# Performance work log

Hardware: AMD Instinct MI355X
Metric: run time of the kernel (lower is better)

Reference implementation:

```python
import jax, jax.numpy as jnp
import numpy as np

N = 4096   # number of observations
Q = 1024   # number of spatial locations (dist_matrix side)


def setup_inputs() -> dict:
    key = jax.random.key(0)
    k1, k2, k3, k4 = jax.random.split(key, 4)
    y_true = jax.random.normal(k1, (N, 1), dtype=jnp.float32)
    y_pred = jax.random.normal(k2, (N, 1), dtype=jnp.float32)
    Z_idx = jax.random.randint(k3, (N, 1), 0, Q).astype(jnp.int64)
    # symmetric distance matrix from random 2D coordinates
    coords = jax.random.uniform(k4, (Q, 2), dtype=jnp.float32) * 10.0
    diff = coords[:, None, :] - coords[None, :, :]
    dist_matrix = jnp.sqrt(jnp.sum(diff * diff, axis=-1) + 1e-12)
    sig2e = jnp.asarray(1.0, dtype=jnp.float32)
    sig2bs = jnp.ones((2,), dtype=jnp.float32)
    return {"y_true": y_true, "y_pred": y_pred, "Z_idx": Z_idx,
            "dist_matrix": dist_matrix, "sig2e": sig2e, "sig2bs": sig2bs}


def reference(y_true, y_pred, Z_idx, dist_matrix, sig2e, sig2bs):
    # NLL for the 'spatial' mixed-effects mode (custom_loss_lm).
    # V = sig2e*I + Z D Z^T with Z the one-hot indicator of Z_idx and
    # D[a,b] = sig2bs[0]*exp(-dist[a,b]/(2*sig2bs[1])).
    # Z D Z^T for one-hot Z is simply the row/col gather D[idx][:, idx],
    # which avoids materializing the dense N x Q indicator matrix.
    n = y_true.shape[0]
    idx = Z_idx[:, 0]
    D = sig2bs[0] * jnp.exp(-dist_matrix / (2.0 * sig2bs[1]))   # (Q, Q)
    V = sig2e * jnp.eye(n, dtype=jnp.float32) + D[idx][:, idx]  # (N, N)
    r = y_true - y_pred                                          # (N, 1)
    V_inv_r = jnp.linalg.solve(V, r)                             # (N, 1)
    quad = jnp.sum(r * V_inv_r)
    _, logdet = jnp.linalg.slogdet(V)
    log2pi = jnp.asarray(np.log(2.0 * np.pi), dtype=jnp.float32)
    total_loss = 0.5 * n * log2pi + 0.5 * logdet + 0.5 * quad
    return total_loss
```

## Files before the change

### kernel.cpp

```cpp
#include <hip/hip_runtime.h>
#include <math.h>

#define NN 4096
#define QQ 1024
#define LDA 1032
#define AF (1025 * 1032)

__global__ void k_stats(const float* __restrict__ yt, const float* __restrict__ yp,
                        const int* __restrict__ idx, float* __restrict__ s,
                        int* __restrict__ c, float* __restrict__ scal) {
    int i = blockIdx.x * 256 + threadIdx.x;
    float r = yt[i] - yp[i];
    int q = idx[i];
    atomicAdd(&s[q], r);
    atomicAdd(&c[q], 1);
    float v = r * r;
    for (int o = 32; o > 0; o >>= 1) v += __shfl_down(v, o, 64);
    __shared__ float red[4];
    int lane = threadIdx.x & 63, wid = threadIdx.x >> 6;
    if (lane == 0) red[wid] = v;
    __syncthreads();
    if (threadIdx.x == 0) atomicAdd(&scal[0], red[0] + red[1] + red[2] + red[3]);
}

__global__ void k_matvec(const float* __restrict__ dist, const float* __restrict__ s,
                         const int* __restrict__ c, float* __restrict__ t,
                         float* __restrict__ w, float* __restrict__ sqc,
                         float* __restrict__ scal, const float* __restrict__ sbs) {
    int i = blockIdx.x;
    float sb0 = sbs[0];
    float inv2 = 1.0f / (2.0f * sbs[1]);
    const float* dr = dist + (size_t)i * QQ;
    float acc = 0.f;
    for (int j = threadIdx.x; j < QQ; j += 256)
        acc += __expf(-dr[j] * inv2) * s[j];
    for (int o = 32; o > 0; o >>= 1) acc += __shfl_down(acc, o, 64);
    __shared__ float red[4];
    int lane = threadIdx.x & 63, wid = threadIdx.x >> 6;
    if (lane == 0) red[wid] = acc;
    __syncthreads();
    if (threadIdx.x == 0) {
        float tot = (red[0] + red[1] + red[2] + red[3]) * sb0;
        t[i] = tot;
        float sq = sqrtf((float)c[i]);
        sqc[i] = sq;
        w[i] = sq * tot;
        atomicAdd(&scal[1], s[i] * tot);
    }
}

__global__ void k_build(const float* __restrict__ dist, const float* __restrict__ sqc,
                        const float* __restrict__ w, float* __restrict__ A,
                        const float* __restrict__ se_p, const float* __restrict__ sbs) {
    int i = blockIdx.x;
    if (i == QQ) {
        for (int j = threadIdx.x; j < QQ; j += 256) A[(size_t)QQ * LDA + j] = w[j];
        return;
    }
    float sb0 = sbs[0];
    float inv2 = 1.0f / (2.0f * sbs[1]);
    float inv_se = 1.0f / se_p[0];
    float qi = sqc[i] * inv_se * sb0;
    const float* dr = dist + (size_t)i * QQ;
    float* ar = A + (size_t)i * LDA;
    for (int j = threadIdx.x; j < QQ; j += 256)
        ar[j] = ((i == j) ? 1.0f : 0.0f) + qi * sqc[j] * __expf(-dr[j] * inv2);
}

__global__ __launch_bounds__(256) void k_potrf(float* __restrict__ A, int p) {
    __shared__ float col[2][64];
    int tid = threadIdx.x;
    int i = tid & 63;
    int q = tid >> 6;
    float* base = A + (size_t)(p * 64 + i) * LDA + p * 64 + 16 * q;
    float x[16];
#pragma unroll
    for (int m4 = 0; m4 < 4; ++m4) {
        float4 v = ((const float4*)base)[m4];
        x[4 * m4 + 0] = v.x; x[4 * m4 + 1] = v.y;
        x[4 * m4 + 2] = v.z; x[4 * m4 + 3] = v.w;
    }
#pragma unroll
    for (int qk = 0; qk < 4; ++qk) {
#pragma unroll
        for (int ck = 0; ck < 16; ++ck) {
            const int k = qk * 16 + ck;
            const int b = k & 1;
            if (q == qk) {
                float xk = x[ck];
                float diag = __shfl(xk, k, 64);
                float rs = rsqrtf(diag);
                float l = (i == k) ? diag * rs : xk * rs;
                if (i >= k) x[ck] = l;
                col[b][i] = l;
            }
            __syncthreads();
            if (16 * q + 15 > k) {
                if (i > k) {
                    float li = col[b][i];
                    float cl[16];
#pragma unroll
                    for (int m4 = 0; m4 < 4; ++m4) {
                        float4 v = ((const float4*)(&col[b][16 * q]))[m4];
                        cl[4 * m4 + 0] = v.x; cl[4 * m4 + 1] = v.y;
                        cl[4 * m4 + 2] = v.z; cl[4 * m4 + 3] = v.w;
                    }
#pragma unroll
                    for (int m = 0; m < 16; ++m)
                        if (16 * q + m > k) x[m] = fmaf(-li, cl[m], x[m]);
                }
            }
        }
    }
#pragma unroll
    for (int m4 = 0; m4 < 4; ++m4)
        ((float4*)base)[m4] = make_float4(x[4 * m4 + 0], x[4 * m4 + 1],
                                          x[4 * m4 + 2], x[4 * m4 + 3]);
}

template<int K, int M>
struct TAcc {
    static __device__ __forceinline__ void run(const float (&Lb)[64][65], const float (&x)[64],
                                               float& a0, float& a1) {
        if constexpr (M < K)     a0 = fmaf(-Lb[K][M], x[M], a0);
        if constexpr (M + 1 < K) a1 = fmaf(-Lb[K][M + 1], x[M + 1], a1);
        if constexpr (M + 2 < K) TAcc<K, M + 2>::run(Lb, x, a0, a1);
    }
};
template<int K>
struct TStep {
    static __device__ __forceinline__ void run(const float (&Lb)[64][65], const float (&dinv)[64],
                                               float (&x)[64]) {
        if constexpr (K < 64) {
            float a0 = x[K], a1 = 0.f;
            TAcc<K, 0>::run(Lb, x, a0, a1);
            x[K] = (a0 + a1) * dinv[K];
            TStep<K + 1>::run(Lb, dinv, x);
        }
    }
};

__global__ __launch_bounds__(64, 2) void k_trsm(float* __restrict__ A, int p) {
    __shared__ float Lb[64][65];
    __shared__ float dinv[64];
    int t = threadIdx.x;
    const float* db = A + (size_t)(p * 64) * (LDA + 1);
    for (int i = 0; i < 64; ++i) Lb[i][t] = db[(size_t)i * LDA + t];
    dinv[t] = 1.0f / Lb[t][t];
    __syncthreads();
    int r = (p + 1) * 64 + blockIdx.x * 64 + t;
    if (r <= QQ) {
        float* ar = A + (size_t)r * LDA + p * 64;
        float x[64];
#pragma unroll
        for (int jj = 0; jj < 16; ++jj) {
            float4 v = ((const float4*)ar)[jj];
            x[4 * jj] = v.x; x[4 * jj + 1] = v.y; x[4 * jj + 2] = v.z; x[4 * jj + 3] = v.w;
        }
        TStep<0>::run(Lb, dinv, x);
#pragma unroll
        for (int jj = 0; jj < 16; ++jj)
            ((float4*)ar)[jj] = make_float4(x[4 * jj], x[4 * jj + 1], x[4 * jj + 2], x[4 * jj + 3]);
    }
}

__global__ void k_syrk(float* __restrict__ A, int p) {
    int t0 = (p + 1) * 64;
    int r0 = t0 + blockIdx.y * 32;
    int c0 = t0 + blockIdx.x * 32;
    if (c0 > r0 + 31) return;
    __shared__ float Pr[32][65];
    __shared__ float Pc[32][65];
    int t = threadIdx.x;
    int pc0 = p * 64;
    for (int idx2 = t; idx2 < 2048; idx2 += 256) {
        int i = idx2 >> 6, k = idx2 & 63;
        int rr = r0 + i;
        Pr[i][k] = (rr <= QQ) ? A[(size_t)rr * LDA + pc0 + k] : 0.f;
        int cc = c0 + i;
        Pc[i][k] = (cc < QQ) ? A[(size_t)cc * LDA + pc0 + k] : 0.f;
    }
    __syncthreads();
    int tx = t & 31, ty = t >> 5;
    float acc[4] = {0.f, 0.f, 0.f, 0.f};
#pragma unroll 4
    for (int k = 0; k < 64; ++k) {
        float b = Pc[tx][k];
#pragma unroll
        for (int ii = 0; ii < 4; ++ii)
            acc[ii] = fmaf(Pr[ty + 8 * ii][k], b, acc[ii]);
    }
#pragma unroll
    for (int ii = 0; ii < 4; ++ii) {
        int rr = r0 + ty + 8 * ii, cc = c0 + tx;
        if (rr <= QQ && cc < QQ)
            A[(size_t)rr * LDA + cc] -= acc[ii];
    }
}

__global__ void k_final(const float* __restrict__ A, const float* __restrict__ scal,
                        const float* __restrict__ se_p, float* __restrict__ out) {
    int i = threadIdx.x;
    float v1 = 2.0f * __logf(A[(size_t)i * LDA + i]);
    float yv = A[(size_t)QQ * LDA + i];
    float v2 = yv * yv;
    for (int o = 32; o > 0; o >>= 1) {
        v1 += __shfl_down(v1, o, 64);
        v2 += __shfl_down(v2, o, 64);
    }
    __shared__ float r1[16], r2[16];
    int lane = i & 63, wid = i >> 6;
    if (lane == 0) { r1[wid] = v1; r2[wid] = v2; }
    __syncthreads();
    if (i == 0) {
        float ld = 0.f, yy = 0.f;
        for (int k = 0; k < 16; ++k) { ld += r1[k]; yy += r2[k]; }
        float se = se_p[0], inv = 1.0f / se;
        float rr = scal[0], st = scal[1];
        float quad = rr * inv - inv * inv * (st - inv * yy);
        float logdetV = (float)NN * __logf(se) + ld;
        out[0] = 0.5f * (float)NN * 1.8378770664093453f + 0.5f * logdetV + 0.5f * quad;
    }
}

extern "C" void kernel_launch(void* const* d_in, const int* in_sizes, int n_in,
                              void* d_out, int out_size, void* d_ws, size_t ws_size,
                              hipStream_t stream) {
    const float* yt   = (const float*)d_in[0];
    const float* yp   = (const float*)d_in[1];
    const int*   idx  = (const int*)d_in[2];
    const float* dist = (const float*)d_in[3];
    const float* se   = (const float*)d_in[4];
    const float* sbs  = (const float*)d_in[5];
    float* out = (float*)d_out;

    float* W    = (float*)d_ws;
    float* A    = W;
    int*   c    = (int*)(W + AF);
    float* s    = W + AF + 1024;
    float* scal = W + AF + 2048;
    float* t    = scal + 2;
    float* w    = t + 1024;
    float* sqc  = w + 1024;

    hipMemsetAsync(c, 0, (1024 + 1024 + 2) * sizeof(float), stream);

    k_stats<<<dim3(NN / 256), dim3(256), 0, stream>>>(yt, yp, idx, s, c, scal);
    k_matvec<<<dim3(QQ), dim3(256), 0, stream>>>(dist, s, c, t, w, sqc, scal, sbs);
    k_build<<<dim3(QQ + 1), dim3(256), 0, stream>>>(dist, sqc, w, A, se, sbs);

    for (int p = 0; p < 16; ++p) {
        k_potrf<<<dim3(1), dim3(256), 0, stream>>>(A, p);
        int rows = (QQ + 1) - (p + 1) * 64;
        k_trsm<<<dim3((rows + 63) / 64), dim3(64), 0, stream>>>(A, p);
        int cols = QQ - (p + 1) * 64;
        if (cols > 0) {
            dim3 g((cols + 31) / 32, (rows + 31) / 32);
            k_syrk<<<g, dim3(256), 0, stream>>>(A, p);
        }
    }
    k_final<<<dim3(1), dim3(1024), 0, stream>>>(A, scal, se, out);
}
```

Before: 796.9 us.

## Fuse next diagonal Cholesky factorization into SYRK update and enlarge SYRK tiles

```diff
diff --git a/kernel.cpp b/kernel.cpp
--- a/kernel.cpp
+++ b/kernel.cpp
@@ -67,55 +67,60 @@
         ar[j] = ((i == j) ? 1.0f : 0.0f) + qi * sqc[j] * __expf(-dr[j] * inv2);
 }
 
-__global__ __launch_bounds__(256) void k_potrf(float* __restrict__ A, int p) {
-    __shared__ float col[2][64];
-    int tid = threadIdx.x;
-    int i = tid & 63;
-    int q = tid >> 6;
-    float* base = A + (size_t)(p * 64 + i) * LDA + p * 64 + 16 * q;
-    float x[16];
-#pragma unroll
-    for (int m4 = 0; m4 < 4; ++m4) {
-        float4 v = ((const float4*)base)[m4];
-        x[4 * m4 + 0] = v.x; x[4 * m4 + 1] = v.y;
-        x[4 * m4 + 2] = v.z; x[4 * m4 + 3] = v.w;
-    }
+__device__ __forceinline__ void potrf64_run(float (&x)[16], int i, int q,
+                                            float2 (&col2)[2][64]) {
 #pragma unroll
     for (int qk = 0; qk < 4; ++qk) {
 #pragma unroll
-        for (int ck = 0; ck < 16; ++ck) {
-            const int k = qk * 16 + ck;
-            const int b = k & 1;
+        for (int c2 = 0; c2 < 8; ++c2) {
+            const int k = qk * 16 + 2 * c2;
+            const int ck = 2 * c2;
+            const int b = c2 & 1;
             if (q == qk) {
                 float xk = x[ck];
-                float diag = __shfl(xk, k, 64);
-                float rs = rsqrtf(diag);
-                float l = (i == k) ? diag * rs : xk * rs;
-                if (i >= k) x[ck] = l;
-                col[b][i] = l;
+                float d0 = __shfl(xk, k, 64);
+                float rs0 = rsqrtf(d0);
+                float l0 = (i == k) ? d0 * rs0 : xk * rs0;
+                if (i >= k) x[ck] = l0;
+                float lk1 = __shfl(l0, k + 1, 64);
+                float x1v = fmaf(-l0, lk1, x[ck + 1]);
+                float d1 = __shfl(x1v, k + 1, 64);
+                float rs1 = rsqrtf(d1);
+                float l1 = (i == k + 1) ? d1 * rs1 : x1v * rs1;
+                if (i >= k + 1) x[ck + 1] = l1;
+                col2[b][i] = make_float2(l0, l1);
             }
             __syncthreads();
-            if (16 * q + 15 > k) {
-                if (i > k) {
-                    float li = col[b][i];
-                    float cl[16];
-#pragma unroll
-                    for (int m4 = 0; m4 < 4; ++m4) {
-                        float4 v = ((const float4*)(&col[b][16 * q]))[m4];
-                        cl[4 * m4 + 0] = v.x; cl[4 * m4 + 1] = v.y;
-                        cl[4 * m4 + 2] = v.z; cl[4 * m4 + 3] = v.w;
-                    }
-#pragma unroll
-                    for (int m = 0; m < 16; ++m)
-                        if (16 * q + m > k) x[m] = fmaf(-li, cl[m], x[m]);
+            if (16 * q + 15 > k + 1 && i > k) {
+                float2 lp = col2[b][i];
+                const float4* cp = (const float4*)(&col2[b][16 * q]);
+#pragma unroll
+                for (int m2 = 0; m2 < 8; ++m2) {
+                    float4 v = cp[m2];
+                    if (16 * q + 2 * m2 > k + 1)
+                        x[2 * m2] = fmaf(-lp.x, v.x, fmaf(-lp.y, v.y, x[2 * m2]));
+                    if (16 * q + 2 * m2 + 1 > k + 1)
+                        x[2 * m2 + 1] = fmaf(-lp.x, v.z, fmaf(-lp.y, v.w, x[2 * m2 + 1]));
                 }
             }
         }
     }
+}
+
+__global__ __launch_bounds__(256) void k_potrf0(float* __restrict__ A) {
+    __shared__ float2 col2[2][64];
+    int tid = threadIdx.x, i = tid & 63, q = tid >> 6;
+    float* row = A + (size_t)i * LDA + 16 * q;
+    float x[16];
+#pragma unroll
+    for (int m4 = 0; m4 < 4; ++m4) {
+        float4 v = ((const float4*)row)[m4];
+        x[4 * m4] = v.x; x[4 * m4 + 1] = v.y; x[4 * m4 + 2] = v.z; x[4 * m4 + 3] = v.w;
+    }
+    potrf64_run(x, i, q, col2);
 #pragma unroll
     for (int m4 = 0; m4 < 4; ++m4)
-        ((float4*)base)[m4] = make_float4(x[4 * m4 + 0], x[4 * m4 + 1],
-                                          x[4 * m4 + 2], x[4 * m4 + 3]);
+        ((float4*)row)[m4] = make_float4(x[4 * m4], x[4 * m4 + 1], x[4 * m4 + 2], x[4 * m4 + 3]);
 }
 
 template<int K, int M>
@@ -164,37 +169,89 @@
     }
 }
 
-__global__ void k_syrk(float* __restrict__ A, int p) {
+__global__ __launch_bounds__(256) void k_syrkpotrf(float* __restrict__ A, int p) {
     int t0 = (p + 1) * 64;
-    int r0 = t0 + blockIdx.y * 32;
-    int c0 = t0 + blockIdx.x * 32;
-    if (c0 > r0 + 31) return;
-    __shared__ float Pr[32][65];
-    __shared__ float Pc[32][65];
-    int t = threadIdx.x;
+    int r0 = t0 + blockIdx.y * 64;
+    int c0 = t0 + blockIdx.x * 64;
+    if (c0 > r0) return;
+    bool dfuse = (blockIdx.x == 0 && blockIdx.y == 0);
+    __shared__ __align__(16) float PrRaw[64 * 68];
+    __shared__ __align__(16) float PcRaw[64 * 68];
+    __shared__ float2 col2[2][64];
+    int tid = threadIdx.x;
+    int tx = tid & 15, ty = tid >> 4;
     int pc0 = p * 64;
-    for (int idx2 = t; idx2 < 2048; idx2 += 256) {
-        int i = idx2 >> 6, k = idx2 & 63;
-        int rr = r0 + i;
-        Pr[i][k] = (rr <= QQ) ? A[(size_t)rr * LDA + pc0 + k] : 0.f;
-        int cc = c0 + i;
-        Pc[i][k] = (cc < QQ) ? A[(size_t)cc * LDA + pc0 + k] : 0.f;
-    }
-    __syncthreads();
-    int tx = t & 31, ty = t >> 5;
-    float acc[4] = {0.f, 0.f, 0.f, 0.f};
+    for (int idx2 = tid; idx2 < 1024; idx2 += 256) {
+        int rr = idx2 >> 4, c4 = idx2 & 15;
+        int gr = r0 + rr;
+        float4 v = make_float4(0.f, 0.f, 0.f, 0.f);
+        if (gr <= QQ) v = *(const float4*)(A + (size_t)gr * LDA + pc0 + 4 * c4);
+        *(float4*)(PrRaw + rr * 68 + 4 * c4) = v;
+        if (!dfuse) {
+            float4 u = *(const float4*)(A + (size_t)(c0 + rr) * LDA + pc0 + 4 * c4);
+            *(float4*)(PcRaw + rr * 68 + 4 * c4) = u;
+        }
+    }
+    __syncthreads();
+    const float* PB = dfuse ? PrRaw : PcRaw;
+    float acc[4][4];
+#pragma unroll
+    for (int ii = 0; ii < 4; ++ii)
+#pragma unroll
+        for (int jj = 0; jj < 4; ++jj) acc[ii][jj] = 0.f;
+    float4 ar[4], br[4];
 #pragma unroll 4
-    for (int k = 0; k < 64; ++k) {
-        float b = Pc[tx][k];
+    for (int k4 = 0; k4 < 16; ++k4) {
 #pragma unroll
         for (int ii = 0; ii < 4; ++ii)
-            acc[ii] = fmaf(Pr[ty + 8 * ii][k], b, acc[ii]);
-    }
-#pragma unroll
-    for (int ii = 0; ii < 4; ++ii) {
-        int rr = r0 + ty + 8 * ii, cc = c0 + tx;
-        if (rr <= QQ && cc < QQ)
-            A[(size_t)rr * LDA + cc] -= acc[ii];
+            ar[ii] = *(const float4*)(PrRaw + (ty + 16 * ii) * 68 + 4 * k4);
+#pragma unroll
+        for (int jj = 0; jj < 4; ++jj)
+            br[jj] = *(const float4*)(PB + (tx + 16 * jj) * 68 + 4 * k4);
+#pragma unroll
+        for (int ii = 0; ii < 4; ++ii)
+#pragma unroll
+            for (int jj = 0; jj < 4; ++jj) {
+                acc[ii][jj] = fmaf(ar[ii].x, br[jj].x, acc[ii][jj]);
+                acc[ii][jj] = fmaf(ar[ii].y, br[jj].y, acc[ii][jj]);
+                acc[ii][jj] = fmaf(ar[ii].z, br[jj].z, acc[ii][jj]);
+                acc[ii][jj] = fmaf(ar[ii].w, br[jj].w, acc[ii][jj]);
+            }
+    }
+    if (!dfuse) {
+#pragma unroll
+        for (int ii = 0; ii < 4; ++ii) {
+            int rr = r0 + ty + 16 * ii;
+            if (rr <= QQ) {
+#pragma unroll
+                for (int jj = 0; jj < 4; ++jj) {
+                    float* pa = A + (size_t)rr * LDA + c0 + tx + 16 * jj;
+                    *pa -= acc[ii][jj];
+                }
+            }
+        }
+    } else {
+#pragma unroll
+        for (int ii = 0; ii < 4; ++ii) {
+            int lr = ty + 16 * ii;
+#pragma unroll
+            for (int jj = 0; jj < 4; ++jj) {
+                int lc = tx + 16 * jj;
+                float old = A[(size_t)(r0 + lr) * LDA + c0 + lc];
+                PcRaw[lr * 65 + lc] = old - acc[ii][jj];
+            }
+        }
+        __syncthreads();
+        int i = tid & 63, q = tid >> 6;
+        float x[16];
+#pragma unroll
+        for (int m = 0; m < 16; ++m) x[m] = PcRaw[i * 65 + 16 * q + m];
+        potrf64_run(x, i, q, col2);
+        float* row = A + (size_t)(r0 + i) * LDA + c0 + 16 * q;
+#pragma unroll
+        for (int m4 = 0; m4 < 4; ++m4)
+            ((float4*)row)[m4] = make_float4(x[4 * m4], x[4 * m4 + 1],
+                                             x[4 * m4 + 2], x[4 * m4 + 3]);
     }
 }
 
@@ -249,15 +306,14 @@
     k_matvec<<<dim3(QQ), dim3(256), 0, stream>>>(dist, s, c, t, w, sqc, scal, sbs);
     k_build<<<dim3(QQ + 1), dim3(256), 0, stream>>>(dist, sqc, w, A, se, sbs);
 
-    for (int p = 0; p < 16; ++p) {
-        k_potrf<<<dim3(1), dim3(256), 0, stream>>>(A, p);
+    k_potrf0<<<dim3(1), dim3(256), 0, stream>>>(A);
+    for (int p = 0; p < 15; ++p) {
         int rows = (QQ + 1) - (p + 1) * 64;
         k_trsm<<<dim3((rows + 63) / 64), dim3(64), 0, stream>>>(A, p);
-        int cols = QQ - (p + 1) * 64;
-        if (cols > 0) {
-            dim3 g((cols + 31) / 32, (rows + 31) / 32);
-            k_syrk<<<g, dim3(256), 0, stream>>>(A, p);
-        }
-    }
+        int ncol = (QQ - (p + 1) * 64) / 64;
+        int nr = (rows + 63) / 64;
+        k_syrkpotrf<<<dim3(ncol, nr), dim3(256), 0, stream>>>(A, p);
+    }
+    k_trsm<<<dim3(1), dim3(64), 0, stream>>>(A, 15);
     k_final<<<dim3(1), dim3(1024), 0, stream>>>(A, scal, se, out);
 }
```

Result: faster. 688.4 us (-13.6%).
